# Optimization experiments

Hardware: AMD Instinct MI355X
Metric: run time of the kernel (lower is better)

## Reference

```python
import jax, jax.numpy as jnp
import numpy as np

N, E, D_IN, D_HID, D_OUT = 50000, 800000, 128, 128, 300
BN_EPS = 1e-5


def setup_inputs() -> dict:
    key = jax.random.key(0)
    ks = jax.random.split(key, 10)
    s_in = 1.0 / np.sqrt(D_IN)
    s_hid = 1.0 / np.sqrt(D_HID)
    return {
        "x": jax.random.normal(ks[0], (N, D_IN), jnp.float32),
        "edge_index": jax.random.randint(ks[1], (2, E), 0, N, jnp.int64),
        "Wl": jax.random.normal(ks[2], (D_IN, D_HID), jnp.float32) * s_in,
        "bl": jnp.zeros((D_HID,), jnp.float32),
        "Wr": jax.random.normal(ks[3], (D_IN, D_HID), jnp.float32) * s_in,
        "Wsk": jax.random.normal(ks[4], (D_IN, D_HID), jnp.float32) * s_in,
        "bsk": jnp.zeros((D_HID,), jnp.float32),
        "gamma": jnp.ones((D_HID,), jnp.float32),
        "beta": jnp.zeros((D_HID,), jnp.float32),
        "rmean": jnp.zeros((D_HID,), jnp.float32),
        "rvar": jnp.ones((D_HID,), jnp.float32),
        "Wlo": jax.random.normal(ks[5], (D_HID, D_OUT), jnp.float32) * s_hid,
        "blo": jnp.zeros((D_OUT,), jnp.float32),
        "Wro": jax.random.normal(ks[6], (D_HID, D_OUT), jnp.float32) * s_hid,
    }


def sage_conv(x, src, dst, n_nodes, W_l, b_l, W_r):
    # PyG SAGEConv (aggr='mean'): lin_l(mean_{j in N(i)} x_j) + lin_r(x_i)
    msgs = x[src]                                                 # [E, d] gather
    agg = jax.ops.segment_sum(msgs, dst, num_segments=n_nodes)    # [N, d]
    cnt = jax.ops.segment_sum(jnp.ones((src.shape[0], 1), x.dtype), dst,
                              num_segments=n_nodes)               # [N, 1]
    mean = agg / jnp.maximum(cnt, 1.0)
    return mean @ W_l + b_l + x @ W_r


def reference(x, edge_index, Wl, bl, Wr, Wsk, bsk, gamma, beta, rmean, rvar,
              Wlo, blo, Wro):
    src, dst = edge_index[0], edge_index[1]
    n = x.shape[0]
    # layer 0: conv + skip linear
    h = sage_conv(x, src, dst, n, Wl, bl, Wr) + (x @ Wsk + bsk)
    # BatchNorm1d (eval: running stats)
    h = (h - rmean) * (gamma * jax.lax.rsqrt(rvar + BN_EPS)) + beta
    x_emb = jax.nn.relu(h)                                        # dropout: no-op in eval
    # output conv + log_softmax
    x_out = sage_conv(x_emb, src, dst, n, Wlo, blo, Wro)
    return h, jax.nn.log_softmax(x_out, axis=1)
```

## Files before the change

### kernel.cpp

```cpp
#include <hip/hip_runtime.h>

typedef __attribute__((__ext_vector_type__(8))) __bf16 bf16x8;
typedef __attribute__((__ext_vector_type__(4))) float f32x4;
typedef __attribute__((__ext_vector_type__(2))) float f32x2;
typedef __attribute__((__ext_vector_type__(4))) unsigned int u32x4;

__device__ __forceinline__ float bf2f(unsigned short u) {
    return __uint_as_float(((unsigned int)u) << 16);
}
__device__ __forceinline__ unsigned short f2bf(float f) {
    unsigned int u = __float_as_uint(f);
    u += 0x7FFFu + ((u >> 16) & 1u);
    return (unsigned short)(u >> 16);
}

__device__ __forceinline__ bool low_short_is_bf16like(unsigned int w) {
    unsigned int lo = w & 0xFFFFu;
    if (lo == 0u || lo == 0x8000u) return true;
    unsigned int e = (lo >> 7) & 0xFFu;
    return (e >= 0x6Cu && e <= 0x8Cu);
}
__device__ __forceinline__ int probe_f32(const unsigned int* __restrict__ p) {
    int t = threadIdx.x & 63;
    int cnt = __popcll(__ballot(low_short_is_bf16like(p[t])));
    return (cnt < 32) ? 1 : 0;
}
__device__ __forceinline__ int probe_e64(const unsigned int* __restrict__ ei) {
    int t = threadIdx.x & 63;
    unsigned int o1 = ei[2 * t + 1];
    unsigned int o2 = ei[2 * t + 129];
    return __all((o1 == 0u) && (o2 == 0u)) ? 1 : 0;
}

__global__ __launch_bounds__(256) void k_tobf(
    const void* __restrict__ xv, unsigned short* __restrict__ xbf,
    unsigned int* __restrict__ x8, int* __restrict__ deg,
    long nelem, int n, int tgrid)
{
    if ((int)blockIdx.x >= tgrid) {
        int j = ((int)blockIdx.x - tgrid) * 256 + threadIdx.x;
        if (j < n) deg[j] = 0;
        return;
    }
    int xf32 = probe_f32((const unsigned int*)xv);
    long i = ((long)blockIdx.x * 256 + threadIdx.x) * 8;
    if (i >= nelem) return;
    float f[8];
    if (xf32) {
        const float4* p = (const float4*)((const float*)xv + i);
        float4 v0 = p[0], v1 = p[1];
        f[0] = v0.x; f[1] = v0.y; f[2] = v0.z; f[3] = v0.w;
        f[4] = v1.x; f[5] = v1.y; f[6] = v1.z; f[7] = v1.w;
        u32x4 o;
        o.x = (unsigned int)f2bf(f[0]) | ((unsigned int)f2bf(f[1]) << 16);
        o.y = (unsigned int)f2bf(f[2]) | ((unsigned int)f2bf(f[3]) << 16);
        o.z = (unsigned int)f2bf(f[4]) | ((unsigned int)f2bf(f[5]) << 16);
        o.w = (unsigned int)f2bf(f[6]) | ((unsigned int)f2bf(f[7]) << 16);
        *(u32x4*)&xbf[i] = o;
    } else {
        u32x4 v = *(const u32x4*)((const unsigned short*)xv + i);
        *(u32x4*)&xbf[i] = v;
        f[0] = bf2f((unsigned short)v.x); f[1] = bf2f((unsigned short)(v.x >> 16));
        f[2] = bf2f((unsigned short)v.y); f[3] = bf2f((unsigned short)(v.y >> 16));
        f[4] = bf2f((unsigned short)v.z); f[5] = bf2f((unsigned short)(v.z >> 16));
        f[6] = bf2f((unsigned short)v.w); f[7] = bf2f((unsigned short)(v.w >> 16));
    }
    unsigned int q0 = 0, q1 = 0;
    q0 = (unsigned int)__builtin_amdgcn_cvt_pk_fp8_f32(f[0], f[1], (int)q0, false);
    q0 = (unsigned int)__builtin_amdgcn_cvt_pk_fp8_f32(f[2], f[3], (int)q0, true);
    q1 = (unsigned int)__builtin_amdgcn_cvt_pk_fp8_f32(f[4], f[5], (int)q1, false);
    q1 = (unsigned int)__builtin_amdgcn_cvt_pk_fp8_f32(f[6], f[7], (int)q1, true);
    uint2 q; q.x = q0; q.y = q1;
    *(uint2*)&x8[i >> 2] = q;
}

__global__ __launch_bounds__(256) void k_fold(
    const void* __restrict__ Wl, const void* __restrict__ Wr,
    const void* __restrict__ Wsk, const void* __restrict__ gamma,
    const void* __restrict__ rvar, const void* __restrict__ bl,
    const void* __restrict__ bsk, const void* __restrict__ rmean,
    const void* __restrict__ beta, const void* __restrict__ Wlo,
    const void* __restrict__ blo, const void* __restrict__ Wro,
    unsigned short* __restrict__ W1p, unsigned short* __restrict__ W2p,
    float* __restrict__ bias1, float* __restrict__ bias2)
{
    int wf32 = probe_f32((const unsigned int*)Wl);
    int b = blockIdx.x, t = threadIdx.x;
    if (b < 128) {
        int idx = b * 256 + t;
        int kb = idx >> 10, c = (idx >> 3) & 127, k7 = idx & 7;
        int k = kb * 8 + k7;
        float g, rv, w;
        if (wf32) {
            g  = ((const float*)gamma)[c];
            rv = ((const float*)rvar)[c];
            if (k < 128) w = ((const float*)Wl)[k * 128 + c];
            else { int kk = k - 128;
                   w = ((const float*)Wr)[kk * 128 + c] + ((const float*)Wsk)[kk * 128 + c]; }
        } else {
            g  = bf2f(((const unsigned short*)gamma)[c]);
            rv = bf2f(((const unsigned short*)rvar)[c]);
            if (k < 128) w = bf2f(((const unsigned short*)Wl)[k * 128 + c]);
            else { int kk = k - 128;
                   w = bf2f(((const unsigned short*)Wr)[kk * 128 + c]) +
                       bf2f(((const unsigned short*)Wsk)[kk * 128 + c]); }
        }
        float s = g * rsqrtf(rv + 1e-5f);
        W1p[idx] = f2bf(w * s);
    } else if (b < 448) {
        int idx = (b - 128) * 256 + t;
        int kb = idx / 2560;
        int rem = idx - kb * 2560;
        int c = rem >> 3, k7 = idx & 7;
        int k = kb * 8 + k7;
        float w = 0.f;
        if (c < 300) {
            if (wf32)
                w = (k < 128) ? ((const float*)Wlo)[k * 300 + c]
                              : ((const float*)Wro)[(k - 128) * 300 + c];
            else
                w = (k < 128) ? bf2f(((const unsigned short*)Wlo)[k * 300 + c])
                              : bf2f(((const unsigned short*)Wro)[(k - 128) * 300 + c]);
        }
        W2p[idx] = f2bf(w);
    } else {
        if (t < 128) {
            float g, rv, b1, b2, rm, be;
            if (wf32) {
                g = ((const float*)gamma)[t]; rv = ((const float*)rvar)[t];
                b1 = ((const float*)bl)[t];   b2 = ((const float*)bsk)[t];
                rm = ((const float*)rmean)[t]; be = ((const float*)beta)[t];
            } else {
                g = bf2f(((const unsigned short*)gamma)[t]); rv = bf2f(((const unsigned short*)rvar)[t]);
                b1 = bf2f(((const unsigned short*)bl)[t]);   b2 = bf2f(((const unsigned short*)bsk)[t]);
                rm = bf2f(((const unsigned short*)rmean)[t]); be = bf2f(((const unsigned short*)beta)[t]);
            }
            float s = g * rsqrtf(rv + 1e-5f);
            bias1[t] = (b1 + b2 - rm) * s + be;
        }
        for (int c = t; c < 320; c += 256) {
            float v = 0.f;
            if (c < 300)
                v = wf32 ? ((const float*)blo)[c] : bf2f(((const unsigned short*)blo)[c]);
            bias2[c] = v;
        }
    }
}

__global__ __launch_bounds__(256) void k_rank(
    const int* __restrict__ ei,
    int* __restrict__ deg, int* __restrict__ rank, int E, int nnodes)
{
    int e64 = probe_e64((const unsigned int*)ei);
    int e = blockIdx.x * 256 + threadIdx.x;
    if (e >= E) return;
    int d = e64 ? ei[2 * (E + e)] : ei[E + e];
    int r = 0;
    if ((unsigned)d < (unsigned)nnodes) r = atomicAdd(&deg[d], 1);
    rank[e] = r;
}

template <typename IT>
__global__ __launch_bounds__(256) void k_place(
    const int* __restrict__ ei,
    const int* __restrict__ rowptr, const int* __restrict__ aux,
    const int* __restrict__ rank,
    IT* __restrict__ adj, int E, int nnodes)
{
    int e64 = probe_e64((const unsigned int*)ei);
    int e = blockIdx.x * 256 + threadIdx.x;
    if (e >= E) return;
    int s, d;
    if (e64) { s = ei[2 * e]; d = ei[2 * (E + e)]; }
    else     { s = ei[e];     d = ei[E + e]; }
    if ((unsigned)d >= (unsigned)nnodes) return;
    if ((unsigned)s >= (unsigned)nnodes) s = 0;
    adj[rowptr[d] + aux[d >> 10] + rank[e]] = (IT)s;
}

__global__ __launch_bounds__(256) void k_scan_a(
    const int* __restrict__ deg, int* __restrict__ rowptr,
    int* __restrict__ aux, int n)
{
    __shared__ int wsum[4];
    int t = threadIdx.x, blk = blockIdx.x;
    int base = blk * 1024 + t * 4;
    int v[4];
    int s = 0;
    #pragma unroll
    for (int i = 0; i < 4; i++) { int idx = base + i; v[i] = (idx < n) ? deg[idx] : 0; s += v[i]; }
    int lane = t & 63, wv = t >> 6;
    int inc = s;
    #pragma unroll
    for (int off = 1; off < 64; off <<= 1) {
        int u = __shfl_up(inc, off);
        if (lane >= off) inc += u;
    }
    if (lane == 63) wsum[wv] = inc;
    __syncthreads();
    int woff = 0;
    if (wv >= 1) woff += wsum[0];
    if (wv >= 2) woff += wsum[1];
    if (wv >= 3) woff += wsum[2];
    int exc = woff + inc - s;
    #pragma unroll
    for (int i = 0; i < 4; i++) { int idx = base + i; if (idx < n) rowptr[idx] = exc; exc += v[i]; }
    if (t == 255) aux[blk] = woff + inc;
}

__global__ __launch_bounds__(64) void k_scan_b(int* __restrict__ aux, int nblk)
{
    int t = threadIdx.x;
    int carry = 0;
    for (int base = 0; base < nblk; base += 64) {
        int idx = base + t;
        int v = (idx < nblk) ? aux[idx] : 0;
        int inc = v;
        #pragma unroll
        for (int off = 1; off < 64; off <<= 1) {
            int u = __shfl_up(inc, off);
            if (t >= off) inc += u;
        }
        if (idx < nblk) aux[idx] = carry + inc - v;
        carry += __shfl(inc, 63);
    }
}

template <typename IT>
__global__ __launch_bounds__(256) void k_agg(
    const unsigned int* __restrict__ x8,
    const int* __restrict__ rowptr, const int* __restrict__ aux,
    const int* __restrict__ deg,
    const IT* __restrict__ adj, unsigned short* __restrict__ meanB, int n)
{
    int wid = (blockIdx.x * 256 + threadIdx.x) >> 6;
    if (wid >= n) return;
    int lane = threadIdx.x & 63;
    int h  = lane >> 5;
    int sl = lane & 31;
    int start = rowptr[wid] + aux[wid >> 10];
    int dc = deg[wid];
    float acc[4][4];
    #pragma unroll
    for (int u = 0; u < 4; u++)
        #pragma unroll
        for (int c = 0; c < 4; c++) acc[u][c] = 0.f;
    int i = 0;
    for (; i + 15 < dc; i += 16) {
        int e[8]; unsigned int p[8];
        #pragma unroll
        for (int u = 0; u < 8; u++) e[u] = (int)adj[start + i + 2 * u + h];
        #pragma unroll
        for (int u = 0; u < 8; u++) p[u] = x8[(size_t)e[u] * 32 + sl];
        #pragma unroll
        for (int u = 0; u < 8; u++) {
            f32x2 lo = __builtin_amdgcn_cvt_pk_f32_fp8((int)p[u], false);
            f32x2 hi = __builtin_amdgcn_cvt_pk_f32_fp8((int)p[u], true);
            acc[u & 3][0] += lo.x; acc[u & 3][1] += lo.y;
            acc[u & 3][2] += hi.x; acc[u & 3][3] += hi.y;
        }
    }
    if (i + 7 < dc) {
        int e[4]; unsigned int p[4];
        #pragma unroll
        for (int u = 0; u < 4; u++) e[u] = (int)adj[start + i + 2 * u + h];
        #pragma unroll
        for (int u = 0; u < 4; u++) p[u] = x8[(size_t)e[u] * 32 + sl];
        #pragma unroll
        for (int u = 0; u < 4; u++) {
            f32x2 lo = __builtin_amdgcn_cvt_pk_f32_fp8((int)p[u], false);
            f32x2 hi = __builtin_amdgcn_cvt_pk_f32_fp8((int)p[u], true);
            acc[u][0] += lo.x; acc[u][1] += lo.y;
            acc[u][2] += hi.x; acc[u][3] += hi.y;
        }
        i += 8;
    }
    for (; i + h < dc; i += 2) {
        int e0 = (int)adj[start + i + h];
        unsigned int p0 = x8[(size_t)e0 * 32 + sl];
        f32x2 lo = __builtin_amdgcn_cvt_pk_f32_fp8((int)p0, false);
        f32x2 hi = __builtin_amdgcn_cvt_pk_f32_fp8((int)p0, true);
        acc[0][0] += lo.x; acc[0][1] += lo.y; acc[0][2] += hi.x; acc[0][3] += hi.y;
    }
    float t0 = (acc[0][0] + acc[1][0]) + (acc[2][0] + acc[3][0]);
    float t1 = (acc[0][1] + acc[1][1]) + (acc[2][1] + acc[3][1]);
    float t2 = (acc[0][2] + acc[1][2]) + (acc[2][2] + acc[3][2]);
    float t3 = (acc[0][3] + acc[1][3]) + (acc[2][3] + acc[3][3]);
    t0 += __shfl_xor(t0, 32);
    t1 += __shfl_xor(t1, 32);
    t2 += __shfl_xor(t2, 32);
    t3 += __shfl_xor(t3, 32);
    if (h == 0) {
        float inv = 1.f / fmaxf((float)dc, 1.f);
        uint2 o;
        o.x = (unsigned int)f2bf(t0 * inv) | ((unsigned int)f2bf(t1 * inv) << 16);
        o.y = (unsigned int)f2bf(t2 * inv) | ((unsigned int)f2bf(t3 * inv) << 16);
        *(uint2*)&meanB[(size_t)wid * 128 + sl * 4] = o;
    }
}

__global__ __launch_bounds__(256) void k_gemm1(
    const unsigned short* __restrict__ meanB,
    const unsigned short* __restrict__ xbf, const unsigned int* __restrict__ xprobe,
    const unsigned short* __restrict__ Wp,
    const float* __restrict__ bias, void* __restrict__ outh,
    unsigned short* __restrict__ xemb, unsigned int* __restrict__ xemb8, int nrows)
{
    constexpr int NTW = 2;
    __shared__ __align__(16) unsigned short Alds[32 * 264];
    int tid = threadIdx.x;
    int row0 = blockIdx.x * 32;
    int xf32 = probe_f32(xprobe);
    {
        int r = tid >> 3, c0 = (tid & 7) * 16;
        int rg = row0 + r; if (rg >= nrows) rg = nrows - 1;
        const u32x4* mp = (const u32x4*)(meanB + (size_t)rg * 128 + c0);
        *(u32x4*)&Alds[r * 264 + c0]     = mp[0];
        *(u32x4*)&Alds[r * 264 + c0 + 8] = mp[1];
        const u32x4* xp = (const u32x4*)(xbf + (size_t)rg * 128 + c0);
        *(u32x4*)&Alds[r * 264 + 128 + c0]     = xp[0];
        *(u32x4*)&Alds[r * 264 + 128 + c0 + 8] = xp[1];
    }
    __syncthreads();
    f32x4 acc[2][NTW];
    #pragma unroll
    for (int a = 0; a < 2; a++)
        #pragma unroll
        for (int b = 0; b < NTW; b++) acc[a][b] = f32x4{0.f, 0.f, 0.f, 0.f};
    int lane = tid & 63, wv = tid >> 6, lh = lane & 15, lq = lane >> 4;
    #pragma unroll
    for (int ks = 0; ks < 8; ++ks) {
        bf16x8 a0 = *(const bf16x8*)&Alds[lh * 264 + ks * 32 + lq * 8];
        bf16x8 a1 = *(const bf16x8*)&Alds[(16 + lh) * 264 + ks * 32 + lq * 8];
        #pragma unroll
        for (int i = 0; i < NTW; i++) {
            int col = (wv + 4 * i) * 16 + lh;
            bf16x8 bfr = *(const bf16x8*)&Wp[(ks * 4 + lq) * 1024 + col * 8];
            acc[0][i] = __builtin_amdgcn_mfma_f32_16x16x32_bf16(a0, bfr, acc[0][i], 0, 0, 0);
            acc[1][i] = __builtin_amdgcn_mfma_f32_16x16x32_bf16(a1, bfr, acc[1][i], 0, 0, 0);
        }
    }
    __syncthreads();
    float* outF = (float*)outh;
    unsigned short* outB = (unsigned short*)outh;
    #pragma unroll
    for (int rt = 0; rt < 2; ++rt)
        #pragma unroll
        for (int i = 0; i < NTW; i++)
            #pragma unroll
            for (int j = 0; j < 4; j++) {
                int rl = rt * 16 + lq * 4 + j;
                int r = row0 + rl;
                int c = (wv + 4 * i) * 16 + lh;
                float v = acc[rt][i][j] + bias[c];
                float rv = fmaxf(v, 0.f);
                unsigned short rb = f2bf(rv);
                Alds[rl * 264 + c] = rb;
                if (r < nrows) {
                    if (xf32) __builtin_nontemporal_store(v, &outF[(size_t)r * 128 + c]);
                    else      outB[(size_t)r * 128 + c] = f2bf(v);
                    xemb[(size_t)r * 128 + c] = rb;
                }
            }
    __syncthreads();
    {
        int r = tid >> 3, c0 = (tid & 7) * 16;
        int rg = row0 + r;
        if (rg < nrows) {
            u32x4 va = *(u32x4*)&Alds[r * 264 + c0];
            u32x4 vb = *(u32x4*)&Alds[r * 264 + c0 + 8];
            u32x4 q;
            unsigned int w;
            w = 0;
            w = (unsigned int)__builtin_amdgcn_cvt_pk_fp8_f32(
                    bf2f((unsigned short)va.x), bf2f((unsigned short)(va.x >> 16)), (int)w, false);
            w = (unsigned int)__builtin_amdgcn_cvt_pk_fp8_f32(
                    bf2f((unsigned short)va.y), bf2f((unsigned short)(va.y >> 16)), (int)w, true);
            q.x = w;
            w = 0;
            w = (unsigned int)__builtin_amdgcn_cvt_pk_fp8_f32(
                    bf2f((unsigned short)va.z), bf2f((unsigned short)(va.z >> 16)), (int)w, false);
            w = (unsigned int)__builtin_amdgcn_cvt_pk_fp8_f32(
                    bf2f((unsigned short)va.w), bf2f((unsigned short)(va.w >> 16)), (int)w, true);
            q.y = w;
            w = 0;
            w = (unsigned int)__builtin_amdgcn_cvt_pk_fp8_f32(
                    bf2f((unsigned short)vb.x), bf2f((unsigned short)(vb.x >> 16)), (int)w, false);
            w = (unsigned int)__builtin_amdgcn_cvt_pk_fp8_f32(
                    bf2f((unsigned short)vb.y), bf2f((unsigned short)(vb.y >> 16)), (int)w, true);
            q.z = w;
            w = 0;
            w = (unsigned int)__builtin_amdgcn_cvt_pk_fp8_f32(
                    bf2f((unsigned short)vb.z), bf2f((unsigned short)(vb.z >> 16)), (int)w, false);
            w = (unsigned int)__builtin_amdgcn_cvt_pk_fp8_f32(
                    bf2f((unsigned short)vb.w), bf2f((unsigned short)(vb.w >> 16)), (int)w, true);
            q.w = w;
            *(u32x4*)&xemb8[(size_t)rg * 32 + (tid & 7) * 4] = q;
        }
    }
}

__global__ __launch_bounds__(256) void k_gemm2(
    const unsigned short* __restrict__ meanB,
    const unsigned short* __restrict__ xf, const unsigned int* __restrict__ xprobe,
    const unsigned short* __restrict__ Wp,
    const float* __restrict__ bias, void* __restrict__ outbase, int nrows)
{
    constexpr int NTW = 5;
    __shared__ __align__(16) unsigned short Alds[32 * 264];
    __shared__ float redM[4][32];
    __shared__ float redS[4][32];
    int tid = threadIdx.x;
    int row0 = blockIdx.x * 32;
    int xf32 = probe_f32(xprobe);
    {
        int r = tid >> 3, c0 = (tid & 7) * 16;
        int rg = row0 + r; if (rg >= nrows) rg = nrows - 1;
        const u32x4* mp = (const u32x4*)(meanB + (size_t)rg * 128 + c0);
        *(u32x4*)&Alds[r * 264 + c0]     = mp[0];
        *(u32x4*)&Alds[r * 264 + c0 + 8] = mp[1];
        const u32x4* xp = (const u32x4*)(xf + (size_t)rg * 128 + c0);
        *(u32x4*)&Alds[r * 264 + 128 + c0]     = xp[0];
        *(u32x4*)&Alds[r * 264 + 128 + c0 + 8] = xp[1];
    }
    __syncthreads();
    f32x4 acc[2][NTW];
    #pragma unroll
    for (int a = 0; a < 2; a++)
        #pragma unroll
        for (int b = 0; b < NTW; b++) acc[a][b] = f32x4{0.f, 0.f, 0.f, 0.f};
    int lane = tid & 63, wv = tid >> 6, lh = lane & 15, lq = lane >> 4;
    #pragma unroll
    for (int ks = 0; ks < 8; ++ks) {
        bf16x8 a0 = *(const bf16x8*)&Alds[lh * 264 + ks * 32 + lq * 8];
        bf16x8 a1 = *(const bf16x8*)&Alds[(16 + lh) * 264 + ks * 32 + lq * 8];
        #pragma unroll
        for (int i = 0; i < NTW; i++) {
            int col = (wv + 4 * i) * 16 + lh;
            bf16x8 bfr = *(const bf16x8*)&Wp[(ks * 4 + lq) * 2560 + col * 8];
            acc[0][i] = __builtin_amdgcn_mfma_f32_16x16x32_bf16(a0, bfr, acc[0][i], 0, 0, 0);
            acc[1][i] = __builtin_amdgcn_mfma_f32_16x16x32_bf16(a1, bfr, acc[1][i], 0, 0, 0);
        }
    }
    #pragma unroll
    for (int rt = 0; rt < 2; ++rt)
        #pragma unroll
        for (int i = 0; i < NTW; i++) {
            int col = (wv + 4 * i) * 16 + lh;
            float b = bias[col];
            #pragma unroll
            for (int j = 0; j < 4; j++) acc[rt][i][j] += b;
        }
    float M[2][4];
    #pragma unroll
    for (int rt = 0; rt < 2; ++rt)
        #pragma unroll
        for (int j = 0; j < 4; j++) {
            float m = -3.0e38f;
            #pragma unroll
            for (int i = 0; i < NTW; i++) {
                int col = (wv + 4 * i) * 16 + lh;
                if (col < 300) m = fmaxf(m, acc[rt][i][j]);
            }
            m = fmaxf(m, __shfl_xor(m, 1, 16));
            m = fmaxf(m, __shfl_xor(m, 2, 16));
            m = fmaxf(m, __shfl_xor(m, 4, 16));
            m = fmaxf(m, __shfl_xor(m, 8, 16));
            M[rt][j] = m;
        }
    if (lh == 0) {
        #pragma unroll
        for (int rt = 0; rt < 2; ++rt)
            #pragma unroll
            for (int j = 0; j < 4; j++)
                redM[wv][rt * 16 + lq * 4 + j] = M[rt][j];
    }
    __syncthreads();
    #pragma unroll
    for (int rt = 0; rt < 2; ++rt)
        #pragma unroll
        for (int j = 0; j < 4; j++) {
            int rl = rt * 16 + lq * 4 + j;
            M[rt][j] = fmaxf(fmaxf(redM[0][rl], redM[1][rl]),
                             fmaxf(redM[2][rl], redM[3][rl]));
        }
    float S[2][4];
    #pragma unroll
    for (int rt = 0; rt < 2; ++rt)
        #pragma unroll
        for (int j = 0; j < 4; j++) {
            float s = 0.f;
            #pragma unroll
            for (int i = 0; i < NTW; i++) {
                int col = (wv + 4 * i) * 16 + lh;
                if (col < 300) s += __expf(acc[rt][i][j] - M[rt][j]);
            }
            s += __shfl_xor(s, 1, 16);
            s += __shfl_xor(s, 2, 16);
            s += __shfl_xor(s, 4, 16);
            s += __shfl_xor(s, 8, 16);
            S[rt][j] = s;
        }
    if (lh == 0) {
        #pragma unroll
        for (int rt = 0; rt < 2; ++rt)
            #pragma unroll
            for (int j = 0; j < 4; j++)
                redS[wv][rt * 16 + lq * 4 + j] = S[rt][j];
    }
    __syncthreads();
    float* out1F = (float*)outbase + (size_t)nrows * 128;
    unsigned short* out1B = (unsigned short*)outbase + (size_t)nrows * 128;
    #pragma unroll
    for (int rt = 0; rt < 2; ++rt)
        #pragma unroll
        for (int j = 0; j < 4; j++) {
            int rl = rt * 16 + lq * 4 + j;
            float Sall = (redS[0][rl] + redS[1][rl]) + (redS[2][rl] + redS[3][rl]);
            float L = M[rt][j] + __logf(Sall);
            int rg = row0 + rl;
            if (rg < nrows) {
                #pragma unroll
                for (int i = 0; i < NTW; i++) {
                    int col = (wv + 4 * i) * 16 + lh;
                    if (col < 300) {
                        float v = acc[rt][i][j] - L;
                        if (xf32) __builtin_nontemporal_store(v, &out1F[(size_t)rg * 300 + col]);
                        else      out1B[(size_t)rg * 300 + col] = f2bf(v);
                    }
                }
            }
        }
}

extern "C" void kernel_launch(void* const* d_in, const int* in_sizes, int n_in,
                              void* d_out, int out_size, void* d_ws, size_t ws_size,
                              hipStream_t stream)
{
    const void* x     = d_in[0];
    const int*  ei    = (const int*)d_in[1];
    const void* Wl    = d_in[2];
    const void* bl    = d_in[3];
    const void* Wr    = d_in[4];
    const void* Wsk   = d_in[5];
    const void* bsk   = d_in[6];
    const void* gamma = d_in[7];
    const void* beta  = d_in[8];
    const void* rmean = d_in[9];
    const void* rvar  = d_in[10];
    const void* Wlo   = d_in[11];
    const void* blo   = d_in[12];
    const void* Wro   = d_in[13];

    int N = in_sizes[0] / 128;
    int E = in_sizes[1] / 2;
    long nelem = (long)N * 128;
    bool idx16 = (N <= 65535);

    char* ws = (char*)d_ws;
    size_t off = 0;
    unsigned short* xbf   = (unsigned short*)(ws + off); off += (size_t)N * 128 * 2;
    unsigned short* meanB = (unsigned short*)(ws + off); off += (size_t)N * 128 * 2;
    unsigned short* xemb  = (unsigned short*)(ws + off); off += (size_t)N * 128 * 2;
    unsigned int* x8      = (unsigned int*)(ws + off);   off += (size_t)N * 128;
    unsigned int* xemb8   = (unsigned int*)(ws + off);   off += (size_t)N * 128;
    off = (off + 255) & ~(size_t)255;
    int* deg    = (int*)(ws + off);           off += (size_t)N * 4;
    int* rowptr = (int*)(ws + off);           off += (size_t)N * 4;
    int* rank   = (int*)(ws + off);           off += (size_t)E * 4;
    int* aux    = (int*)(ws + off);           off += 256;
    void* adjv  = (void*)(ws + off);          off += (size_t)E * 4;
    off = (off + 255) & ~(size_t)255;
    unsigned short* W1p = (unsigned short*)(ws + off);  off += 32768 * 2;
    unsigned short* W2p = (unsigned short*)(ws + off);  off += 81920 * 2;
    float* bias1 = (float*)(ws + off);        off += 512;
    float* bias2 = (float*)(ws + off);        off += 1280;

    int egrid = (E + 255) / 256;
    int sblk  = (N + 1023) / 1024;
    int agrid = (N + 3) / 4;
    int ggrid = (N + 31) / 32;
    int tgrid = (int)((nelem / 8 + 255) / 256);
    int dgrid = (N + 255) / 256;

    const unsigned int* xprobe = (const unsigned int*)x;

    k_tobf<<<tgrid + dgrid, 256, 0, stream>>>(x, xbf, x8, deg, nelem, N, tgrid);
    k_fold<<<449, 256, 0, stream>>>(Wl, Wr, Wsk, gamma, rvar, bl, bsk, rmean, beta,
                                    Wlo, blo, Wro, W1p, W2p, bias1, bias2);

    k_rank<<<egrid, 256, 0, stream>>>(ei, deg, rank, E, N);
    k_scan_a<<<sblk, 256, 0, stream>>>(deg, rowptr, aux, N);
    k_scan_b<<<1, 64, 0, stream>>>(aux, sblk);

    if (idx16) {
        unsigned short* adj = (unsigned short*)adjv;
        k_place<unsigned short><<<egrid, 256, 0, stream>>>(ei, rowptr, aux, rank, adj, E, N);
        k_agg<unsigned short><<<agrid, 256, 0, stream>>>(x8, rowptr, aux, deg, adj, meanB, N);
        k_gemm1<<<ggrid, 256, 0, stream>>>(meanB, xbf, xprobe, W1p, bias1, d_out, xemb, xemb8, N);
        k_agg<unsigned short><<<agrid, 256, 0, stream>>>(xemb8, rowptr, aux, deg, adj, meanB, N);
        k_gemm2<<<ggrid, 256, 0, stream>>>(meanB, xemb, xprobe, W2p, bias2, d_out, N);
    } else {
        int* adj = (int*)adjv;
        k_place<int><<<egrid, 256, 0, stream>>>(ei, rowptr, aux, rank, adj, E, N);
        k_agg<int><<<agrid, 256, 0, stream>>>(x8, rowptr, aux, deg, adj, meanB, N);
        k_gemm1<<<ggrid, 256, 0, stream>>>(meanB, xbf, xprobe, W1p, bias1, d_out, xemb, xemb8, N);
        k_agg<int><<<agrid, 256, 0, stream>>>(xemb8, rowptr, aux, deg, adj, meanB, N);
        k_gemm2<<<ggrid, 256, 0, stream>>>(meanB, xemb, xprobe, W2p, bias2, d_out, N);
    }
}
```

Measured before the change: 179.6 us.

## Pack edge endpoints in rank pass, prefetch GEMM weights, drop nontemporal stores

k_rank now also reads the source index and writes a packed 32-bit (dst,src) word per edge, so k_place16 reads 4 bytes per edge instead of re-reading the int64 edge_index. Both GEMM kernels software-prefetch the next k-step's weight fragments into registers before issuing the current MFMAs, aiming to hide global-load latency. The log_softmax output store switches from nontemporal to a normal store. The trade-offs are an extra E*4 workspace write, more register pressure in the GEMMs, and possible cache pollution from the output stores.

```diff
diff --git a/kernel.cpp b/kernel.cpp
--- a/kernel.cpp
+++ b/kernel.cpp
@@ -149,23 +149,42 @@
 
 __global__ __launch_bounds__(256) void k_rank(
     const int* __restrict__ ei,
-    int* __restrict__ deg, int* __restrict__ rank, int E, int nnodes)
+    int* __restrict__ deg, int* __restrict__ rank,
+    unsigned int* __restrict__ ds32, int E, int nnodes, int pack)
 {
     int e64 = probe_e64((const unsigned int*)ei);
     int e = blockIdx.x * 256 + threadIdx.x;
     if (e >= E) return;
-    int d = e64 ? ei[2 * (E + e)] : ei[E + e];
+    int s, d;
+    if (e64) { s = ei[2 * e]; d = ei[2 * (E + e)]; }
+    else     { s = ei[e];     d = ei[E + e]; }
+    if ((unsigned)s >= (unsigned)nnodes) s = 0;
     int r = 0;
     if ((unsigned)d < (unsigned)nnodes) r = atomicAdd(&deg[d], 1);
     rank[e] = r;
-}
-
-template <typename IT>
-__global__ __launch_bounds__(256) void k_place(
+    if (pack) ds32[e] = (((unsigned int)d & 0xFFFFu) << 16) | ((unsigned int)s & 0xFFFFu);
+}
+
+__global__ __launch_bounds__(256) void k_place16(
+    const unsigned int* __restrict__ ds32,
+    const int* __restrict__ rowptr, const int* __restrict__ aux,
+    const int* __restrict__ rank,
+    unsigned short* __restrict__ adj, int E, int nnodes)
+{
+    int e = blockIdx.x * 256 + threadIdx.x;
+    if (e >= E) return;
+    unsigned int ds = ds32[e];
+    int d = (int)(ds >> 16);
+    unsigned short s = (unsigned short)(ds & 0xFFFFu);
+    if (d >= nnodes) return;
+    adj[rowptr[d] + aux[d >> 10] + rank[e]] = s;
+}
+
+__global__ __launch_bounds__(256) void k_place32(
     const int* __restrict__ ei,
     const int* __restrict__ rowptr, const int* __restrict__ aux,
     const int* __restrict__ rank,
-    IT* __restrict__ adj, int E, int nnodes)
+    int* __restrict__ adj, int E, int nnodes)
 {
     int e64 = probe_e64((const unsigned int*)ei);
     int e = blockIdx.x * 256 + threadIdx.x;
@@ -175,7 +194,7 @@
     else     { s = ei[e];     d = ei[E + e]; }
     if ((unsigned)d >= (unsigned)nnodes) return;
     if ((unsigned)s >= (unsigned)nnodes) s = 0;
-    adj[rowptr[d] + aux[d >> 10] + rank[e]] = (IT)s;
+    adj[rowptr[d] + aux[d >> 10] + rank[e]] = s;
 }
 
 __global__ __launch_bounds__(256) void k_scan_a(
@@ -328,17 +347,26 @@
         #pragma unroll
         for (int b = 0; b < NTW; b++) acc[a][b] = f32x4{0.f, 0.f, 0.f, 0.f};
     int lane = tid & 63, wv = tid >> 6, lh = lane & 15, lq = lane >> 4;
+    bf16x8 bcur[NTW], bnxt[NTW];
+    #pragma unroll
+    for (int i = 0; i < NTW; i++)
+        bcur[i] = *(const bf16x8*)&Wp[lq * 1024 + ((wv + 4 * i) * 16 + lh) * 8];
     #pragma unroll
     for (int ks = 0; ks < 8; ++ks) {
+        if (ks < 7) {
+            #pragma unroll
+            for (int i = 0; i < NTW; i++)
+                bnxt[i] = *(const bf16x8*)&Wp[((ks + 1) * 4 + lq) * 1024 + ((wv + 4 * i) * 16 + lh) * 8];
+        }
         bf16x8 a0 = *(const bf16x8*)&Alds[lh * 264 + ks * 32 + lq * 8];
         bf16x8 a1 = *(const bf16x8*)&Alds[(16 + lh) * 264 + ks * 32 + lq * 8];
         #pragma unroll
         for (int i = 0; i < NTW; i++) {
-            int col = (wv + 4 * i) * 16 + lh;
-            bf16x8 bfr = *(const bf16x8*)&Wp[(ks * 4 + lq) * 1024 + col * 8];
-            acc[0][i] = __builtin_amdgcn_mfma_f32_16x16x32_bf16(a0, bfr, acc[0][i], 0, 0, 0);
-            acc[1][i] = __builtin_amdgcn_mfma_f32_16x16x32_bf16(a1, bfr, acc[1][i], 0, 0, 0);
-        }
+            acc[0][i] = __builtin_amdgcn_mfma_f32_16x16x32_bf16(a0, bcur[i], acc[0][i], 0, 0, 0);
+            acc[1][i] = __builtin_amdgcn_mfma_f32_16x16x32_bf16(a1, bcur[i], acc[1][i], 0, 0, 0);
+        }
+        #pragma unroll
+        for (int i = 0; i < NTW; i++) bcur[i] = bnxt[i];
     }
     __syncthreads();
     float* outF = (float*)outh;
@@ -430,17 +458,26 @@
         #pragma unroll
         for (int b = 0; b < NTW; b++) acc[a][b] = f32x4{0.f, 0.f, 0.f, 0.f};
     int lane = tid & 63, wv = tid >> 6, lh = lane & 15, lq = lane >> 4;
+    bf16x8 bcur[NTW], bnxt[NTW];
+    #pragma unroll
+    for (int i = 0; i < NTW; i++)
+        bcur[i] = *(const bf16x8*)&Wp[lq * 2560 + ((wv + 4 * i) * 16 + lh) * 8];
     #pragma unroll
     for (int ks = 0; ks < 8; ++ks) {
+        if (ks < 7) {
+            #pragma unroll
+            for (int i = 0; i < NTW; i++)
+                bnxt[i] = *(const bf16x8*)&Wp[((ks + 1) * 4 + lq) * 2560 + ((wv + 4 * i) * 16 + lh) * 8];
+        }
         bf16x8 a0 = *(const bf16x8*)&Alds[lh * 264 + ks * 32 + lq * 8];
         bf16x8 a1 = *(const bf16x8*)&Alds[(16 + lh) * 264 + ks * 32 + lq * 8];
         #pragma unroll
         for (int i = 0; i < NTW; i++) {
-            int col = (wv + 4 * i) * 16 + lh;
-            bf16x8 bfr = *(const bf16x8*)&Wp[(ks * 4 + lq) * 2560 + col * 8];
-            acc[0][i] = __builtin_amdgcn_mfma_f32_16x16x32_bf16(a0, bfr, acc[0][i], 0, 0, 0);
-            acc[1][i] = __builtin_amdgcn_mfma_f32_16x16x32_bf16(a1, bfr, acc[1][i], 0, 0, 0);
-        }
+            acc[0][i] = __builtin_amdgcn_mfma_f32_16x16x32_bf16(a0, bcur[i], acc[0][i], 0, 0, 0);
+            acc[1][i] = __builtin_amdgcn_mfma_f32_16x16x32_bf16(a1, bcur[i], acc[1][i], 0, 0, 0);
+        }
+        #pragma unroll
+        for (int i = 0; i < NTW; i++) bcur[i] = bnxt[i];
     }
     #pragma unroll
     for (int rt = 0; rt < 2; ++rt)
@@ -525,7 +562,7 @@
                     int col = (wv + 4 * i) * 16 + lh;
                     if (col < 300) {
                         float v = acc[rt][i][j] - L;
-                        if (xf32) __builtin_nontemporal_store(v, &out1F[(size_t)rg * 300 + col]);
+                        if (xf32) out1F[(size_t)rg * 300 + col] = v;
                         else      out1B[(size_t)rg * 300 + col] = f2bf(v);
                     }
                 }
@@ -568,6 +605,7 @@
     int* deg    = (int*)(ws + off);           off += (size_t)N * 4;
     int* rowptr = (int*)(ws + off);           off += (size_t)N * 4;
     int* rank   = (int*)(ws + off);           off += (size_t)E * 4;
+    unsigned int* ds32 = (unsigned int*)(ws + off); off += (size_t)E * 4;
     int* aux    = (int*)(ws + off);           off += 256;
     void* adjv  = (void*)(ws + off);          off += (size_t)E * 4;
     off = (off + 255) & ~(size_t)255;
@@ -589,20 +627,20 @@
     k_fold<<<449, 256, 0, stream>>>(Wl, Wr, Wsk, gamma, rvar, bl, bsk, rmean, beta,
                                     Wlo, blo, Wro, W1p, W2p, bias1, bias2);
 
-    k_rank<<<egrid, 256, 0, stream>>>(ei, deg, rank, E, N);
+    k_rank<<<egrid, 256, 0, stream>>>(ei, deg, rank, ds32, E, N, idx16 ? 1 : 0);
     k_scan_a<<<sblk, 256, 0, stream>>>(deg, rowptr, aux, N);
     k_scan_b<<<1, 64, 0, stream>>>(aux, sblk);
 
     if (idx16) {
         unsigned short* adj = (unsigned short*)adjv;
-        k_place<unsigned short><<<egrid, 256, 0, stream>>>(ei, rowptr, aux, rank, adj, E, N);
+        k_place16<<<egrid, 256, 0, stream>>>(ds32, rowptr, aux, rank, adj, E, N);
         k_agg<unsigned short><<<agrid, 256, 0, stream>>>(x8, rowptr, aux, deg, adj, meanB, N);
         k_gemm1<<<ggrid, 256, 0, stream>>>(meanB, xbf, xprobe, W1p, bias1, d_out, xemb, xemb8, N);
         k_agg<unsigned short><<<agrid, 256, 0, stream>>>(xemb8, rowptr, aux, deg, adj, meanB, N);
         k_gemm2<<<ggrid, 256, 0, stream>>>(meanB, xemb, xprobe, W2p, bias2, d_out, N);
     } else {
         int* adj = (int*)adjv;
-        k_place<int><<<egrid, 256, 0, stream>>>(ei, rowptr, aux, rank, adj, E, N);
+        k_place32<<<egrid, 256, 0, stream>>>(ei, rowptr, aux, rank, adj, E, N);
         k_agg<int><<<agrid, 256, 0, stream>>>(x8, rowptr, aux, deg, adj, meanB, N);
         k_gemm1<<<ggrid, 256, 0, stream>>>(meanB, xbf, xprobe, W1p, bias1, d_out, xemb, xemb8, N);
         k_agg<int><<<agrid, 256, 0, stream>>>(xemb8, rowptr, aux, deg, adj, meanB, N);
```

Measured after the change: 171.3 us. 4.6% less time.
